# Kernel tuning notes

Hardware: AMD Instinct MI355X
Metric: run time of the kernel (lower is better)

Reference implementation:

```python
import jax, jax.numpy as jnp
import numpy as np

B, T, V, F, O, K_ORDER = 16, 16, 512, 64, 64, 3


def setup_inputs() -> dict:
    key = jax.random.key(0)
    k1, k2, k3, k4 = jax.random.split(key, 4)
    x = jax.random.normal(k1, (B, T, V, F), dtype=jnp.float32)
    Att = jax.random.uniform(k2, (B, V, V), dtype=jnp.float32)
    S = jax.random.uniform(k3, (B, T, V, V), dtype=jnp.float32)
    Theta = jax.random.uniform(k4, (K_ORDER, F, O), dtype=jnp.float32) * 0.1
    return {"x": x, "Att": Att, "S": S, "Theta": Theta}


def reference(x, Att, S, Theta):
    # x: (B,T,V,F); Att: (B,V,V); S: (B,T,V,V); Theta: (k,F,O)
    Bv, Tv, Vv, Fv = x.shape
    k_order = Theta.shape[0]
    # symmetrize via elementwise min with transpose over the two vertex dims
    S = jnp.minimum(S, jnp.swapaxes(S, -1, -2))
    # per-timestep: D = diag(sum(A, axis=1)) (sum over rows, i.e. axis=2 here)
    deg = S.sum(axis=2)                      # (B,T,V)
    eye = jnp.eye(Vv, dtype=x.dtype)
    # L_t = D - A - I
    L_t = deg[..., None] * eye - S - eye     # (B,T,V,V)
    Att_b = Att[:, None]                     # (B,1,V,V) broadcast over T

    # Chebyshev recurrence is ELEMENTWISE in the original code: T_k = 2*L_t*T_{k-1} - T_{k-2}
    Tkm2 = jnp.broadcast_to(eye, L_t.shape)  # T_0 = I
    Tkm1 = L_t                               # T_1 = L_t
    # rhs = (T_k * Att)^T @ x  ->  sum_u (T_k*Att)[u,v] * x[u,f]; then @ Theta[k]
    out = jnp.einsum('btuv,btuf,fo->btvo', Tkm2 * Att_b, x, Theta[0])
    if k_order > 1:
        out = out + jnp.einsum('btuv,btuf,fo->btvo', Tkm1 * Att_b, x, Theta[1])
    for i in range(2, k_order):
        Tk = 2.0 * L_t * Tkm1 - Tkm2
        out = out + jnp.einsum('btuv,btuf,fo->btvo', Tk * Att_b, x, Theta[i])
        Tkm2, Tkm1 = Tkm1, Tk
    return jax.nn.relu(out)                  # (B,T,V,O)
```

## Files before the change

kernel.cpp:

```cpp
#include <hip/hip_runtime.h>

#define VV 512
#define FF 64
#define OO 64
#define YELEMS 8388608

using f32x4 = __attribute__((ext_vector_type(4))) float;
using s16x8 = __attribute__((ext_vector_type(8))) short;
using u16x4 = __attribute__((ext_vector_type(4))) unsigned short;

__device__ __forceinline__ short f2bf(float f) {
    union { float f; unsigned int u; } v; v.f = f;
    unsigned int u = v.u;
    u += 0x7fffu + ((u >> 16) & 1u);
    return (short)(u >> 16);
}
__device__ __forceinline__ float bf2f(unsigned short u) {
    union { unsigned int u; float f; } v; v.u = ((unsigned int)u) << 16; return v.f;
}

__device__ __forceinline__ int swz(int row) { return (row >> 1) & 7; }

__global__ __launch_bounds__(256, 4)
void y_kernel(const float* __restrict__ x, const float* __restrict__ Theta,
              unsigned short* __restrict__ yT)
{
    __shared__ __align__(16) unsigned char smem[32768];
    short* xT = (short*)(smem);

    const int tid = threadIdx.x, lane = tid & 63, q = tid >> 6;
    const int g = lane >> 4, nbase = lane & 15;
    const int bt = blockIdx.x >> 3;
    const int u0 = (blockIdx.x & 7) * 64;

    {
        const float* xp = x + ((size_t)(bt * VV + u0 + lane)) * FF + q * 16;
        float4 a0 = ((const float4*)xp)[0];
        float4 a1 = ((const float4*)xp)[1];
        float4 a2 = ((const float4*)xp)[2];
        float4 a3 = ((const float4*)xp)[3];
        float v[16] = {a0.x,a0.y,a0.z,a0.w, a1.x,a1.y,a1.z,a1.w,
                       a2.x,a2.y,a2.z,a2.w, a3.x,a3.y,a3.z,a3.w};
        s16x8 p0, p1;
        #pragma unroll
        for (int e = 0; e < 8; ++e) { p0[e] = f2bf(v[e]); p1[e] = f2bf(v[8 + e]); }
        const int fs = swz(lane);
        *(s16x8*)&xT[lane * 64 + (((q * 2)     ^ fs) * 8)] = p0;
        *(s16x8*)&xT[lane * 64 + (((q * 2 + 1) ^ fs) * 8)] = p1;
    }
    #pragma unroll
    for (int k = 0; k < 3; ++k) {
        short* tk = (short*)(smem + 8192 + k * 8192);
        s16x8 p0, p1;
        #pragma unroll
        for (int e = 0; e < 8; ++e) {
            p0[e] = f2bf(Theta[k * FF * OO + (q * 16 + e) * OO + lane]);
            p1[e] = f2bf(Theta[k * FF * OO + (q * 16 + 8 + e) * OO + lane]);
        }
        const int fs = swz(lane);
        *(s16x8*)&tk[lane * 64 + (((q * 2)     ^ fs) * 8)] = p0;
        *(s16x8*)&tk[lane * 64 + (((q * 2 + 1) ^ fs) * 8)] = p1;
    }
    __syncthreads();

    f32x4 zero = {0.f, 0.f, 0.f, 0.f};
    f32x4 acc[3][4];
    #pragma unroll
    for (int k = 0; k < 3; ++k)
        #pragma unroll
        for (int nt = 0; nt < 4; ++nt) acc[k][nt] = zero;

    const int mrow = q * 16 + nbase;
    const int moff = mrow * 64, ms = swz(mrow);
    #pragma unroll
    for (int kk = 0; kk < 2; ++kk) {
        const int slotA = kk * 4 + g;
        s16x8 a = *(const s16x8*)&xT[moff + ((slotA ^ ms) * 8)];
        #pragma unroll
        for (int nt = 0; nt < 4; ++nt) {
            const int nrow = nt * 16 + nbase;
            const int nad = nrow * 64 + ((slotA ^ swz(nrow)) * 8);
            #pragma unroll
            for (int k = 0; k < 3; ++k) {
                s16x8 b = *(const s16x8*)&((short*)(smem + 8192 + k * 8192))[nad];
                acc[k][nt] = __builtin_amdgcn_mfma_f32_16x16x32_bf16(a, b, acc[k][nt], 0, 0, 0);
            }
        }
    }
    #pragma unroll
    for (int k = 0; k < 3; ++k) {
        #pragma unroll
        for (int nt = 0; nt < 4; ++nt) {
            const int o = nt * 16 + nbase;
            const int u = u0 + q * 16 + g * 4;
            u16x4 pk;
            #pragma unroll
            for (int r = 0; r < 4; ++r) pk[r] = (unsigned short)f2bf(acc[k][nt][r]);
            *(u16x4*)&yT[(size_t)k * YELEMS + ((size_t)(bt * 64 + o)) * VV + u] = pk;
        }
    }
}

__global__ __launch_bounds__(256, 4)
void cheb_main(const float* __restrict__ S, const float* __restrict__ Att,
               const unsigned short* __restrict__ yT, float* __restrict__ out)
{
    __shared__ __align__(16) unsigned char smem[35584];
    short* cT1 = (short*)(smem);
    short* cT2 = (short*)(smem + 8192);
    short* yL1 = (short*)(smem + 16384);
    short* yL2 = (short*)(smem + 24576);
    float* degpart = (float*)(smem + 32768);
    float* degv    = (float*)(smem + 34816);
    float* Adg     = (float*)(smem + 35072);
    float* Sdg     = (float*)(smem + 35328);

    const int tid = threadIdx.x, lane = tid & 63, q = tid >> 6;
    const int nbase = lane & 15, g = lane >> 4;

    const int wg = blockIdx.x;
    const int bt = (wg & 7) + ((wg >> 6) << 3);
    const int vt = (wg >> 3) & 7;
    const int v0 = vt * 64;
    const int b  = bt >> 4;

    const float* Sbt = S + (size_t)bt * VV * VV;
    const float* Abt = Att + (size_t)b * VV * VV;
    const unsigned short* y0g = yT + (size_t)bt * 64 * VV;
    const unsigned short* y1g = y0g + (size_t)YELEMS;
    const unsigned short* y2g = y0g + (size_t)2 * YELEMS;

    const int vb   = (lane & 31) * 2;
    const int sIdx = q + ((lane >> 5) << 2);
    const int yrow  = q * 8 + (lane >> 3);
    const int yslot = lane & 7;

    f32x4 zero = {0.f, 0.f, 0.f, 0.f};
    f32x4 acc1[4], acc2[4];
    #pragma unroll
    for (int i = 0; i < 4; ++i) { acc1[i] = zero; acc2[i] = zero; }
    float dega = 0.f, degb = 0.f;

    const int mrow = q * 16 + nbase;
    const int moff = mrow * 64, ms = swz(mrow);

    for (int ut = 0; ut < 8; ++ut) {
        const int u0t = ut * 64;
        const int ub  = u0t + sIdx * 8;
        const float* sra = Sbt + (size_t)(v0 + vb) * VV + ub;
        float4 ra0 = ((const float4*)sra)[0], ra1 = ((const float4*)sra)[1];
        const float* srb = sra + VV;
        float4 rb0 = ((const float4*)srb)[0], rb1 = ((const float4*)srb)[1];
        float rowa[8] = {ra0.x,ra0.y,ra0.z,ra0.w, ra1.x,ra1.y,ra1.z,ra1.w};
        float rowb[8] = {rb0.x,rb0.y,rb0.z,rb0.w, rb1.x,rb1.y,rb1.z,rb1.w};

        s16x8 p1a, p1b, p2a, p2b;
        #pragma unroll
        for (int e = 0; e < 8; ++e) {
            const int ug = ub + e;
            float2 sc = *(const float2*)&Sbt[(size_t)ug * VV + v0 + vb];
            float2 av = *(const float2*)&Abt[(size_t)ug * VV + v0 + vb];
            float sma = fminf(sc.x, rowa[e]);
            float smb = fminf(sc.y, rowb[e]);
            dega += sma; degb += smb;
            float c1a = -av.x * sma, c1b = -av.y * smb;
            float c2a = 2.0f * av.x * sma * sma, c2b = 2.0f * av.y * smb * smb;
            if (ug == v0 + vb)     { c1a = 0.f; c2a = 0.f; Adg[vb]     = av.x; Sdg[vb]     = sma; }
            if (ug == v0 + vb + 1) { c1b = 0.f; c2b = 0.f; Adg[vb + 1] = av.y; Sdg[vb + 1] = smb; }
            p1a[e] = f2bf(c1a); p1b[e] = f2bf(c1b);
            p2a[e] = f2bf(c2a); p2b[e] = f2bf(c2b);
        }
        const int sa = ((sIdx ^ swz(vb))     * 8);
        const int sb = ((sIdx ^ swz(vb + 1)) * 8);
        *(s16x8*)&cT1[vb * 64 + sa] = p1a;  *(s16x8*)&cT1[(vb + 1) * 64 + sb] = p1b;
        *(s16x8*)&cT2[vb * 64 + sa] = p2a;  *(s16x8*)&cT2[(vb + 1) * 64 + sb] = p2b;

        #pragma unroll
        for (int p = 0; p < 2; ++p) {
            const int orow = yrow + p * 32;
            const size_t gidx = (size_t)orow * VV + u0t + yslot * 8;
            s16x8 w1 = *(const s16x8*)&y1g[gidx];
            s16x8 w2 = *(const s16x8*)&y2g[gidx];
            const int ad = orow * 64 + ((yslot ^ swz(orow)) * 8);
            *(s16x8*)&yL1[ad] = w1;
            *(s16x8*)&yL2[ad] = w2;
        }
        __syncthreads();

        #pragma unroll
        for (int kk = 0; kk < 2; ++kk) {
            const int slotA = kk * 4 + g;
            s16x8 a1 = *(const s16x8*)&cT1[moff + ((slotA ^ ms) * 8)];
            s16x8 a2 = *(const s16x8*)&cT2[moff + ((slotA ^ ms) * 8)];
            #pragma unroll
            for (int nt = 0; nt < 4; ++nt) {
                const int nrow = nt * 16 + nbase;
                const int nad = nrow * 64 + ((slotA ^ swz(nrow)) * 8);
                s16x8 b1 = *(const s16x8*)&yL1[nad];
                s16x8 b2 = *(const s16x8*)&yL2[nad];
                acc1[nt] = __builtin_amdgcn_mfma_f32_16x16x32_bf16(a1, b1, acc1[nt], 0, 0, 0);
                acc2[nt] = __builtin_amdgcn_mfma_f32_16x16x32_bf16(a2, b2, acc2[nt], 0, 0, 0);
            }
        }
        __syncthreads();
    }

    degpart[sIdx * 64 + vb]     = dega;
    degpart[sIdx * 64 + vb + 1] = degb;
    __syncthreads();
    if (tid < 64) {
        float d = 0.f;
        #pragma unroll
        for (int s = 0; s < 8; ++s) d += degpart[s * 64 + tid];
        degv[tid] = d;
    }
    __syncthreads();

    float* obt = out + (size_t)bt * VV * OO;
    #pragma unroll
    for (int r = 0; r < 4; ++r) {
        const int vloc = q * 16 + g * 4 + r;
        const float Ad = Adg[vloc];
        const float Ld = degv[vloc] - Sdg[vloc] - 1.0f;
        const float w1 = Ad * Ld;
        const float w2 = Ad * (2.0f * Ld * Ld - 1.0f);
        const int vg = v0 + vloc;
        #pragma unroll
        for (int nt = 0; nt < 4; ++nt) {
            const int oo = nt * 16 + nbase;
            const size_t yi = (size_t)oo * VV + vg;
            float y0v = bf2f(y0g[yi]);
            float y1v = bf2f(y1g[yi]);
            float y2v = bf2f(y2g[yi]);
            float val = acc1[nt][r] + acc2[nt][r] + Ad * y0v + w1 * y1v + w2 * y2v;
            obt[(size_t)vg * OO + oo] = fmaxf(val, 0.0f);
        }
    }
}

extern "C" void kernel_launch(void* const* d_in, const int* in_sizes, int n_in,
                              void* d_out, int out_size, void* d_ws, size_t ws_size,
                              hipStream_t stream) {
    (void)in_sizes; (void)n_in; (void)ws_size; (void)out_size;
    const float* x   = (const float*)d_in[0];
    const float* Att = (const float*)d_in[1];
    const float* S   = (const float*)d_in[2];
    const float* Th  = (const float*)d_in[3];
    float* outp = (float*)d_out;
    unsigned short* yT = (unsigned short*)d_ws;
    hipLaunchKernelGGL(y_kernel, dim3(2048), dim3(256), 0, stream, x, Th, yT);
    hipLaunchKernelGGL(cheb_main, dim3(2048), dim3(256), 0, stream, S, Att, yT, outp);
}
```

Before: 235.0 us.

## Prefetch next S/Att tile in registers and stream pre-swizzled y tiles via global_load_lds

y_kernel now writes the order-1 and order-2 projected tiles in a pre-swizzled LDS image layout, so cheb_main can copy them straight into LDS with global_load_lds instead of loading them through registers. cheb_main also loads the next u-tile of S, S-transposed and Att into registers while the current tile is processed, and reorganizes the thread mapping so each thread handles 4x4 blocks. The aim is to hide global latency and cut VGPR traffic for the y staging. The cost is higher register pressure, so launch bounds drop to 3 waves and the degree partial buffer grows.

```diff
diff --git a/kernel.cpp b/kernel.cpp
--- a/kernel.cpp
+++ b/kernel.cpp
@@ -3,10 +3,12 @@
 #define VV 512
 #define FF 64
 #define OO 64
-#define YELEMS 8388608
+#define Y0E 8388608
+#define IMGE 8388608
 
 using f32x4 = __attribute__((ext_vector_type(4))) float;
 using s16x8 = __attribute__((ext_vector_type(8))) short;
+using s16x4 = __attribute__((ext_vector_type(4))) short;
 using u16x4 = __attribute__((ext_vector_type(4))) unsigned short;
 
 __device__ __forceinline__ short f2bf(float f) {
@@ -18,8 +20,13 @@
 __device__ __forceinline__ float bf2f(unsigned short u) {
     union { unsigned int u; float f; } v; v.u = ((unsigned int)u) << 16; return v.f;
 }
-
 __device__ __forceinline__ int swz(int row) { return (row >> 1) & 7; }
+
+__device__ __forceinline__ void gload16(const void* g, void* l) {
+    __builtin_amdgcn_global_load_lds(
+        (const __attribute__((address_space(1))) unsigned int*)g,
+        (__attribute__((address_space(3))) unsigned int*)l, 16, 0, 0);
+}
 
 __global__ __launch_bounds__(256, 4)
 void y_kernel(const float* __restrict__ x, const float* __restrict__ Theta,
@@ -31,7 +38,8 @@
     const int tid = threadIdx.x, lane = tid & 63, q = tid >> 6;
     const int g = lane >> 4, nbase = lane & 15;
     const int bt = blockIdx.x >> 3;
-    const int u0 = (blockIdx.x & 7) * 64;
+    const int utile = blockIdx.x & 7;
+    const int u0 = utile * 64;
 
     {
         const float* xp = x + ((size_t)(bt * VV + u0 + lane)) * FF + q * 16;
@@ -88,32 +96,44 @@
         }
     }
     #pragma unroll
-    for (int k = 0; k < 3; ++k) {
-        #pragma unroll
-        for (int nt = 0; nt < 4; ++nt) {
-            const int o = nt * 16 + nbase;
-            const int u = u0 + q * 16 + g * 4;
-            u16x4 pk;
-            #pragma unroll
-            for (int r = 0; r < 4; ++r) pk[r] = (unsigned short)f2bf(acc[k][nt][r]);
-            *(u16x4*)&yT[(size_t)k * YELEMS + ((size_t)(bt * 64 + o)) * VV + u] = pk;
-        }
-    }
-}
-
-__global__ __launch_bounds__(256, 4)
+    for (int nt = 0; nt < 4; ++nt) {
+        const int o = nt * 16 + nbase;
+        u16x4 p0;
+        #pragma unroll
+        for (int r = 0; r < 4; ++r) p0[r] = (unsigned short)f2bf(acc[0][nt][r]);
+        *(u16x4*)&yT[(size_t)bt * 32768 + (size_t)o * VV + u0 + q * 16 + g * 4] = p0;
+    }
+    unsigned short* im1 = yT + (size_t)Y0E + ((size_t)bt * 8 + utile) * 4096;
+    unsigned short* im2 = im1 + (size_t)IMGE;
+    const int sb = q * 2 + (g >> 1), hf = g & 1;
+    #pragma unroll
+    for (int nt = 0; nt < 4; ++nt) {
+        const int o = nt * 16 + nbase;
+        const int ad = o * 64 + ((sb ^ swz(o)) * 8) + hf * 4;
+        u16x4 p1, p2;
+        #pragma unroll
+        for (int r = 0; r < 4; ++r) {
+            p1[r] = (unsigned short)f2bf(acc[1][nt][r]);
+            p2[r] = (unsigned short)f2bf(acc[2][nt][r]);
+        }
+        *(u16x4*)&im1[ad] = p1;
+        *(u16x4*)&im2[ad] = p2;
+    }
+}
+
+__global__ __launch_bounds__(256, 3)
 void cheb_main(const float* __restrict__ S, const float* __restrict__ Att,
                const unsigned short* __restrict__ yT, float* __restrict__ out)
 {
-    __shared__ __align__(16) unsigned char smem[35584];
+    __shared__ __align__(16) unsigned char smem[37632];
     short* cT1 = (short*)(smem);
     short* cT2 = (short*)(smem + 8192);
     short* yL1 = (short*)(smem + 16384);
     short* yL2 = (short*)(smem + 24576);
     float* degpart = (float*)(smem + 32768);
-    float* degv    = (float*)(smem + 34816);
-    float* Adg     = (float*)(smem + 35072);
-    float* Sdg     = (float*)(smem + 35328);
+    float* degv    = (float*)(smem + 36864);
+    float* Adg     = (float*)(smem + 37120);
+    float* Sdg     = (float*)(smem + 37376);
 
     const int tid = threadIdx.x, lane = tid & 63, q = tid >> 6;
     const int nbase = lane & 15, g = lane >> 4;
@@ -126,67 +146,82 @@
 
     const float* Sbt = S + (size_t)bt * VV * VV;
     const float* Abt = Att + (size_t)b * VV * VV;
-    const unsigned short* y0g = yT + (size_t)bt * 64 * VV;
-    const unsigned short* y1g = y0g + (size_t)YELEMS;
-    const unsigned short* y2g = y0g + (size_t)2 * YELEMS;
-
-    const int vb   = (lane & 31) * 2;
-    const int sIdx = q + ((lane >> 5) << 2);
-    const int yrow  = q * 8 + (lane >> 3);
-    const int yslot = lane & 7;
-
-    f32x4 zero = {0.f, 0.f, 0.f, 0.f};
+    const unsigned short* y0p  = yT + (size_t)bt * 64 * VV;
+    const unsigned short* img1 = yT + (size_t)Y0E + (size_t)bt * 8 * 4096;
+    const unsigned short* img2 = img1 + (size_t)IMGE;
+
+    const int vq   = (lane & 15) * 4;
+    const int tIdx = (lane >> 4) + q * 4;
+
+    f32x4 zero = {0.f,0.f,0.f,0.f};
     f32x4 acc1[4], acc2[4];
     #pragma unroll
     for (int i = 0; i < 4; ++i) { acc1[i] = zero; acc2[i] = zero; }
-    float dega = 0.f, degb = 0.f;
+    float da[4] = {0.f, 0.f, 0.f, 0.f};
 
     const int mrow = q * 16 + nbase;
     const int moff = mrow * 64, ms = swz(mrow);
 
+    f32x4 csc[4], cac[4], csr[4];
+    {
+        const float* sb = Sbt + (size_t)(tIdx * 4) * VV + v0 + vq;
+        const float* ab = Abt + (size_t)(tIdx * 4) * VV + v0 + vq;
+        const float* rb = Sbt + (size_t)(v0 + vq) * VV + tIdx * 4;
+        #pragma unroll
+        for (int e = 0; e < 4; ++e) {
+            csc[e] = *(const f32x4*)(sb + e * VV);
+            cac[e] = *(const f32x4*)(ab + e * VV);
+            csr[e] = *(const f32x4*)(rb + e * VV);
+        }
+    }
+
+    #pragma unroll
     for (int ut = 0; ut < 8; ++ut) {
-        const int u0t = ut * 64;
-        const int ub  = u0t + sIdx * 8;
-        const float* sra = Sbt + (size_t)(v0 + vb) * VV + ub;
-        float4 ra0 = ((const float4*)sra)[0], ra1 = ((const float4*)sra)[1];
-        const float* srb = sra + VV;
-        float4 rb0 = ((const float4*)srb)[0], rb1 = ((const float4*)srb)[1];
-        float rowa[8] = {ra0.x,ra0.y,ra0.z,ra0.w, ra1.x,ra1.y,ra1.z,ra1.w};
-        float rowb[8] = {rb0.x,rb0.y,rb0.z,rb0.w, rb1.x,rb1.y,rb1.z,rb1.w};
-
-        s16x8 p1a, p1b, p2a, p2b;
-        #pragma unroll
-        for (int e = 0; e < 8; ++e) {
-            const int ug = ub + e;
-            float2 sc = *(const float2*)&Sbt[(size_t)ug * VV + v0 + vb];
-            float2 av = *(const float2*)&Abt[(size_t)ug * VV + v0 + vb];
-            float sma = fminf(sc.x, rowa[e]);
-            float smb = fminf(sc.y, rowb[e]);
-            dega += sma; degb += smb;
-            float c1a = -av.x * sma, c1b = -av.y * smb;
-            float c2a = 2.0f * av.x * sma * sma, c2b = 2.0f * av.y * smb * smb;
-            if (ug == v0 + vb)     { c1a = 0.f; c2a = 0.f; Adg[vb]     = av.x; Sdg[vb]     = sma; }
-            if (ug == v0 + vb + 1) { c1b = 0.f; c2b = 0.f; Adg[vb + 1] = av.y; Sdg[vb + 1] = smb; }
-            p1a[e] = f2bf(c1a); p1b[e] = f2bf(c1b);
-            p2a[e] = f2bf(c2a); p2b[e] = f2bf(c2b);
-        }
-        const int sa = ((sIdx ^ swz(vb))     * 8);
-        const int sb = ((sIdx ^ swz(vb + 1)) * 8);
-        *(s16x8*)&cT1[vb * 64 + sa] = p1a;  *(s16x8*)&cT1[(vb + 1) * 64 + sb] = p1b;
-        *(s16x8*)&cT2[vb * 64 + sa] = p2a;  *(s16x8*)&cT2[(vb + 1) * 64 + sb] = p2b;
-
-        #pragma unroll
-        for (int p = 0; p < 2; ++p) {
-            const int orow = yrow + p * 32;
-            const size_t gidx = (size_t)orow * VV + u0t + yslot * 8;
-            s16x8 w1 = *(const s16x8*)&y1g[gidx];
-            s16x8 w2 = *(const s16x8*)&y2g[gidx];
-            const int ad = orow * 64 + ((yslot ^ swz(orow)) * 8);
-            *(s16x8*)&yL1[ad] = w1;
-            *(s16x8*)&yL2[ad] = w2;
+        {
+            const char* t1 = (const char*)img1 + (size_t)ut * 8192;
+            const char* t2 = (const char*)img2 + (size_t)ut * 8192;
+            const int wo = q * 1024 + lane * 16;
+            gload16(t1 + wo,        (char*)yL1 + q * 1024);
+            gload16(t1 + wo + 4096, (char*)yL1 + q * 1024 + 4096);
+            gload16(t2 + wo,        (char*)yL2 + q * 1024);
+            gload16(t2 + wo + 4096, (char*)yL2 + q * 1024 + 4096);
+        }
+        f32x4 nsc[4], nac[4], nsr[4];
+        if (ut < 7) {
+            const int u0n = (ut + 1) * 64;
+            const float* sb = Sbt + (size_t)(u0n + tIdx * 4) * VV + v0 + vq;
+            const float* ab = Abt + (size_t)(u0n + tIdx * 4) * VV + v0 + vq;
+            const float* rb = Sbt + (size_t)(v0 + vq) * VV + u0n + tIdx * 4;
+            #pragma unroll
+            for (int e = 0; e < 4; ++e) {
+                nsc[e] = *(const f32x4*)(sb + e * VV);
+                nac[e] = *(const f32x4*)(ab + e * VV);
+                nsr[e] = *(const f32x4*)(rb + e * VV);
+            }
+        }
+        const bool dtile = (ut == vt);
+        #pragma unroll
+        for (int j = 0; j < 4; ++j) {
+            s16x4 p1, p2;
+            #pragma unroll
+            for (int e = 0; e < 4; ++e) {
+                float sm = fminf(csc[e][j], csr[j][e]);
+                da[j] += sm;
+                float a = cac[e][j];
+                float c1 = -a * sm;
+                float c2 = (a + a) * (sm * sm);
+                if (dtile && (tIdx * 4 + e == vq + j)) {
+                    c1 = 0.f; c2 = 0.f;
+                    Adg[vq + j] = a; Sdg[vq + j] = sm;
+                }
+                p1[e] = f2bf(c1);
+                p2[e] = f2bf(c2);
+            }
+            const int ad = (vq + j) * 64 + (((tIdx >> 1) ^ swz(vq + j)) * 8) + (tIdx & 1) * 4;
+            *(s16x4*)&cT1[ad] = p1;
+            *(s16x4*)&cT2[ad] = p2;
         }
         __syncthreads();
-
         #pragma unroll
         for (int kk = 0; kk < 2; ++kk) {
             const int slotA = kk * 4 + g;
@@ -203,35 +238,41 @@
             }
         }
         __syncthreads();
-    }
-
-    degpart[sIdx * 64 + vb]     = dega;
-    degpart[sIdx * 64 + vb + 1] = degb;
+        if (ut < 7) {
+            #pragma unroll
+            for (int e = 0; e < 4; ++e) { csc[e] = nsc[e]; cac[e] = nac[e]; csr[e] = nsr[e]; }
+        }
+    }
+
+    #pragma unroll
+    for (int j = 0; j < 4; ++j) degpart[tIdx * 64 + vq + j] = da[j];
     __syncthreads();
     if (tid < 64) {
         float d = 0.f;
         #pragma unroll
-        for (int s = 0; s < 8; ++s) d += degpart[s * 64 + tid];
+        for (int s = 0; s < 16; ++s) d += degpart[s * 64 + tid];
         degv[tid] = d;
     }
     __syncthreads();
 
     float* obt = out + (size_t)bt * VV * OO;
+    const unsigned short* t1v = img1 + (size_t)vt * 4096;
+    const unsigned short* t2v = img2 + (size_t)vt * 4096;
     #pragma unroll
     for (int r = 0; r < 4; ++r) {
         const int vloc = q * 16 + g * 4 + r;
+        const int vg = v0 + vloc;
         const float Ad = Adg[vloc];
         const float Ld = degv[vloc] - Sdg[vloc] - 1.0f;
         const float w1 = Ad * Ld;
         const float w2 = Ad * (2.0f * Ld * Ld - 1.0f);
-        const int vg = v0 + vloc;
         #pragma unroll
         for (int nt = 0; nt < 4; ++nt) {
             const int oo = nt * 16 + nbase;
-            const size_t yi = (size_t)oo * VV + vg;
-            float y0v = bf2f(y0g[yi]);
-            float y1v = bf2f(y1g[yi]);
-            float y2v = bf2f(y2g[yi]);
+            const int idx = oo * 64 + (((vloc >> 3) ^ swz(oo)) * 8) + (vloc & 7);
+            float y0v = bf2f(y0p[(size_t)oo * VV + vg]);
+            float y1v = bf2f(t1v[idx]);
+            float y2v = bf2f(t2v[idx]);
             float val = acc1[nt][r] + acc2[nt][r] + Ad * y0v + w1 * y1v + w2 * y2v;
             obt[(size_t)vg * OO + oo] = fmaxf(val, 0.0f);
         }
```

Result: no change. 232.0 us (-1.3%).

## Drop LDS staging in cheb_main, load MFMA operands directly from global memory

Applied to the files above, without the earlier changes.

The main kernel no longer stages the coefficient tiles and y tiles in shared memory. Each lane computes its own A-operand fragment from S row/column and Att column loads and loads the y fragments straight from global memory into registers. This removes both __syncthreads per tile and the LDS round trip. The two accumulators merge into one, and the degree and diagonal reduction uses cross-lane shuffles instead of shared memory. The cost is redundant global reads: every wave reloads the y fragments, and S/Att columns are read as strided scalar loads that are uncoalesced across lanes, which may raise memory traffic and latency.

```diff
diff --git a/kernel.cpp b/kernel.cpp
--- a/kernel.cpp
+++ b/kernel.cpp
@@ -18,7 +18,6 @@
 __device__ __forceinline__ float bf2f(unsigned short u) {
     union { unsigned int u; float f; } v; v.u = ((unsigned int)u) << 16; return v.f;
 }
-
 __device__ __forceinline__ int swz(int row) { return (row >> 1) & 7; }
 
 __global__ __launch_bounds__(256, 4)
@@ -105,18 +104,8 @@
 void cheb_main(const float* __restrict__ S, const float* __restrict__ Att,
                const unsigned short* __restrict__ yT, float* __restrict__ out)
 {
-    __shared__ __align__(16) unsigned char smem[35584];
-    short* cT1 = (short*)(smem);
-    short* cT2 = (short*)(smem + 8192);
-    short* yL1 = (short*)(smem + 16384);
-    short* yL2 = (short*)(smem + 24576);
-    float* degpart = (float*)(smem + 32768);
-    float* degv    = (float*)(smem + 34816);
-    float* Adg     = (float*)(smem + 35072);
-    float* Sdg     = (float*)(smem + 35328);
-
     const int tid = threadIdx.x, lane = tid & 63, q = tid >> 6;
-    const int nbase = lane & 15, g = lane >> 4;
+    const int g = lane >> 4, nbase = lane & 15;
 
     const int wg = blockIdx.x;
     const int bt = (wg & 7) + ((wg >> 6) << 3);
@@ -130,110 +119,84 @@
     const unsigned short* y1g = y0g + (size_t)YELEMS;
     const unsigned short* y2g = y0g + (size_t)2 * YELEMS;
 
-    const int vb   = (lane & 31) * 2;
-    const int sIdx = q + ((lane >> 5) << 2);
-    const int yrow  = q * 8 + (lane >> 3);
-    const int yslot = lane & 7;
+    const int mrow = q * 16 + nbase;
+    const int vg   = v0 + mrow;
+    const float* Srow = Sbt + (size_t)vg * VV;
+    const float* Scol = Sbt + vg;
+    const float* Acol = Abt + vg;
 
     f32x4 zero = {0.f, 0.f, 0.f, 0.f};
-    f32x4 acc1[4], acc2[4];
-    #pragma unroll
-    for (int i = 0; i < 4; ++i) { acc1[i] = zero; acc2[i] = zero; }
-    float dega = 0.f, degb = 0.f;
-
-    const int mrow = q * 16 + nbase;
-    const int moff = mrow * 64, ms = swz(mrow);
+    f32x4 acc[4];
+    #pragma unroll
+    for (int i = 0; i < 4; ++i) acc[i] = zero;
+    float da = 0.f, adg = 0.f, sdg = 0.f;
 
     for (int ut = 0; ut < 8; ++ut) {
         const int u0t = ut * 64;
-        const int ub  = u0t + sIdx * 8;
-        const float* sra = Sbt + (size_t)(v0 + vb) * VV + ub;
-        float4 ra0 = ((const float4*)sra)[0], ra1 = ((const float4*)sra)[1];
-        const float* srb = sra + VV;
-        float4 rb0 = ((const float4*)srb)[0], rb1 = ((const float4*)srb)[1];
-        float rowa[8] = {ra0.x,ra0.y,ra0.z,ra0.w, ra1.x,ra1.y,ra1.z,ra1.w};
-        float rowb[8] = {rb0.x,rb0.y,rb0.z,rb0.w, rb1.x,rb1.y,rb1.z,rb1.w};
-
-        s16x8 p1a, p1b, p2a, p2b;
-        #pragma unroll
-        for (int e = 0; e < 8; ++e) {
-            const int ug = ub + e;
-            float2 sc = *(const float2*)&Sbt[(size_t)ug * VV + v0 + vb];
-            float2 av = *(const float2*)&Abt[(size_t)ug * VV + v0 + vb];
-            float sma = fminf(sc.x, rowa[e]);
-            float smb = fminf(sc.y, rowb[e]);
-            dega += sma; degb += smb;
-            float c1a = -av.x * sma, c1b = -av.y * smb;
-            float c2a = 2.0f * av.x * sma * sma, c2b = 2.0f * av.y * smb * smb;
-            if (ug == v0 + vb)     { c1a = 0.f; c2a = 0.f; Adg[vb]     = av.x; Sdg[vb]     = sma; }
-            if (ug == v0 + vb + 1) { c1b = 0.f; c2b = 0.f; Adg[vb + 1] = av.y; Sdg[vb + 1] = smb; }
-            p1a[e] = f2bf(c1a); p1b[e] = f2bf(c1b);
-            p2a[e] = f2bf(c2a); p2b[e] = f2bf(c2b);
-        }
-        const int sa = ((sIdx ^ swz(vb))     * 8);
-        const int sb = ((sIdx ^ swz(vb + 1)) * 8);
-        *(s16x8*)&cT1[vb * 64 + sa] = p1a;  *(s16x8*)&cT1[(vb + 1) * 64 + sb] = p1b;
-        *(s16x8*)&cT2[vb * 64 + sa] = p2a;  *(s16x8*)&cT2[(vb + 1) * 64 + sb] = p2b;
-
-        #pragma unroll
-        for (int p = 0; p < 2; ++p) {
-            const int orow = yrow + p * 32;
-            const size_t gidx = (size_t)orow * VV + u0t + yslot * 8;
-            s16x8 w1 = *(const s16x8*)&y1g[gidx];
-            s16x8 w2 = *(const s16x8*)&y2g[gidx];
-            const int ad = orow * 64 + ((yslot ^ swz(orow)) * 8);
-            *(s16x8*)&yL1[ad] = w1;
-            *(s16x8*)&yL2[ad] = w2;
-        }
-        __syncthreads();
-
         #pragma unroll
         for (int kk = 0; kk < 2; ++kk) {
-            const int slotA = kk * 4 + g;
-            s16x8 a1 = *(const s16x8*)&cT1[moff + ((slotA ^ ms) * 8)];
-            s16x8 a2 = *(const s16x8*)&cT2[moff + ((slotA ^ ms) * 8)];
+            const int ub = u0t + (kk * 4 + g) * 8;
+            s16x8 b1f[4], b2f[4];
             #pragma unroll
             for (int nt = 0; nt < 4; ++nt) {
-                const int nrow = nt * 16 + nbase;
-                const int nad = nrow * 64 + ((slotA ^ swz(nrow)) * 8);
-                s16x8 b1 = *(const s16x8*)&yL1[nad];
-                s16x8 b2 = *(const s16x8*)&yL2[nad];
-                acc1[nt] = __builtin_amdgcn_mfma_f32_16x16x32_bf16(a1, b1, acc1[nt], 0, 0, 0);
-                acc2[nt] = __builtin_amdgcn_mfma_f32_16x16x32_bf16(a2, b2, acc2[nt], 0, 0, 0);
-            }
-        }
-        __syncthreads();
-    }
-
-    degpart[sIdx * 64 + vb]     = dega;
-    degpart[sIdx * 64 + vb + 1] = degb;
-    __syncthreads();
-    if (tid < 64) {
-        float d = 0.f;
-        #pragma unroll
-        for (int s = 0; s < 8; ++s) d += degpart[s * 64 + tid];
-        degv[tid] = d;
-    }
-    __syncthreads();
+                const size_t yo = (size_t)(nt * 16 + nbase) * VV + ub;
+                b1f[nt] = *(const s16x8*)&y1g[yo];
+                b2f[nt] = *(const s16x8*)&y2g[yo];
+            }
+            f32x4 r0 = *(const f32x4*)(Srow + ub);
+            f32x4 r1 = *(const f32x4*)(Srow + ub + 4);
+            float sc[8], av[8];
+            #pragma unroll
+            for (int e = 0; e < 8; ++e) {
+                sc[e] = Scol[(size_t)(ub + e) * VV];
+                av[e] = Acol[(size_t)(ub + e) * VV];
+            }
+            s16x8 a1, a2;
+            #pragma unroll
+            for (int e = 0; e < 8; ++e) {
+                float rv = (e < 4) ? r0[e] : r1[e - 4];
+                float sm = fminf(sc[e], rv);
+                da += sm;
+                float a = av[e];
+                float c1 = -a * sm;
+                float c2 = (a + a) * (sm * sm);
+                if (ub + e == vg) { c1 = 0.f; c2 = 0.f; adg = a; sdg = sm; }
+                a1[e] = f2bf(c1);
+                a2[e] = f2bf(c2);
+            }
+            #pragma unroll
+            for (int nt = 0; nt < 4; ++nt) {
+                acc[nt] = __builtin_amdgcn_mfma_f32_16x16x32_bf16(a1, b1f[nt], acc[nt], 0, 0, 0);
+                acc[nt] = __builtin_amdgcn_mfma_f32_16x16x32_bf16(a2, b2f[nt], acc[nt], 0, 0, 0);
+            }
+        }
+    }
+
+    da  += __shfl_xor(da, 16);  da  += __shfl_xor(da, 32);
+    adg += __shfl_xor(adg, 16); adg += __shfl_xor(adg, 32);
+    sdg += __shfl_xor(sdg, 16); sdg += __shfl_xor(sdg, 32);
 
     float* obt = out + (size_t)bt * VV * OO;
     #pragma unroll
     for (int r = 0; r < 4; ++r) {
         const int vloc = q * 16 + g * 4 + r;
-        const float Ad = Adg[vloc];
-        const float Ld = degv[vloc] - Sdg[vloc] - 1.0f;
+        const int src  = g * 4 + r;
+        const float Ad = __shfl(adg, src);
+        const float dv = __shfl(da,  src);
+        const float Sd = __shfl(sdg, src);
+        const float Ld = dv - Sd - 1.0f;
         const float w1 = Ad * Ld;
         const float w2 = Ad * (2.0f * Ld * Ld - 1.0f);
-        const int vg = v0 + vloc;
+        const int vgr = v0 + vloc;
         #pragma unroll
         for (int nt = 0; nt < 4; ++nt) {
             const int oo = nt * 16 + nbase;
-            const size_t yi = (size_t)oo * VV + vg;
+            const size_t yi = (size_t)oo * VV + vgr;
             float y0v = bf2f(y0g[yi]);
             float y1v = bf2f(y1g[yi]);
             float y2v = bf2f(y2g[yi]);
-            float val = acc1[nt][r] + acc2[nt][r] + Ad * y0v + w1 * y1v + w2 * y2v;
-            obt[(size_t)vg * OO + oo] = fmaxf(val, 0.0f);
+            float val = acc[nt][r] + Ad * y0v + w1 * y1v + w2 * y2v;
+            obt[(size_t)vgr * OO + oo] = fmaxf(val, 0.0f);
         }
     }
 }
```

Measured after the change: 248.9 us. 1.06x slower.
